# Optimization experiments

Hardware: AMD Instinct MI355X
Metric: run time of the kernel (lower is better)

## Reference

```python
import jax, jax.numpy as jnp
import numpy as np

B, N, L, E, U, G, R, D, C = 64, 50000, 8, 100000, 20000, 20000, 64, 16, 2


def setup_inputs() -> dict:
    rng = np.random.default_rng(0)
    key = jax.random.key(0)
    ks = jax.random.split(key, 10)
    # index structures (duplicate-free where the torch code assumes uniqueness)
    gene_map = jnp.asarray(rng.choice(N, G, replace=False).astype(np.int32))
    dst_unique = jnp.stack([jnp.asarray(rng.choice(N, U, replace=False).astype(np.int32)) for _ in range(L)])
    root_ids = jnp.asarray(rng.choice(N, R, replace=False).astype(np.int32))
    src = jax.random.randint(ks[0], (L, E), 0, N, dtype=jnp.int32)
    dst_pos = jax.random.randint(ks[1], (L, E), 0, U, dtype=jnp.int32)
    # data and parameters
    X_gene_batch = jax.random.normal(ks[2], (B, G), jnp.float32)
    w_in = jax.random.normal(ks[3], (D,), jnp.float32) * 0.5   # Linear(1, d) weight
    b_in = jax.random.normal(ks[4], (D,), jnp.float32) * 0.1
    W = jax.random.normal(ks[5], (L, D, D), jnp.float32) * (1.0 / np.sqrt(D))  # xavier-ish
    bias = jnp.zeros((N, D), jnp.float32)
    W_head = jax.random.normal(ks[6], (C, R * D), jnp.float32) * (1.0 / np.sqrt(R * D))
    b_head = jnp.zeros((C,), jnp.float32)
    return {
        "X_gene_batch": X_gene_batch, "w_in": w_in, "b_in": b_in, "W": W,
        "bias": bias, "W_head": W_head, "b_head": b_head,
        "gene_map": gene_map, "src": src, "dst_pos": dst_pos,
        "dst_unique": dst_unique, "root_ids": root_ids,
    }


def reference(X_gene_batch, w_in, b_in, W, bias, W_head, b_head,
              gene_map, src, dst_pos, dst_unique, root_ids):
    Bn = X_gene_batch.shape[0]
    n_nodes, d = bias.shape
    n_layers = W.shape[0]
    u = dst_unique.shape[1]
    # _init_state_vector: h=0, scatter in_proj(X[...,None]) at gene_map
    gene_emb = X_gene_batch[..., None] * w_in + b_in          # [B, G, d]
    h = jnp.zeros((Bn, n_nodes, d), X_gene_batch.dtype)
    h = h.at[:, gene_map].set(gene_emb)
    for li in range(n_layers):
        h_src = h[:, src[li]]                                  # gather [B, E, d]
        msg = jnp.einsum('bed,df->bef', h_src, W[li])          # small dxd matmul
        agg = jnp.zeros((Bn, u, d), h.dtype).at[:, dst_pos[li]].add(msg)  # scatter-add
        h_dst = jnp.tanh(agg + bias[dst_unique[li]][None])     # bias lookup + tanh (dropout=0)
        h = h.at[:, dst_unique[li]].set(h_dst)                 # write back
    feat = h[:, root_ids].reshape(Bn, -1)                      # roots_concat readout
    return feat @ W_head.T + b_head                            # [B, C]
```

## Files before the change

### kernel.cpp

```cpp
#include <hip/hip_runtime.h>
#include <hip/hip_fp16.h>
#include <cmath>

constexpr int B_ = 64, N_ = 50000, L_ = 8, E_ = 100000, U_ = 20000, G_ = 20000, R_ = 64, D_ = 16, C_ = 2;
constexpr int EPL_ = E_ + 3 * U_ + 4096;
constexpr int EPLG_ = EPL_ / 4 + 64;
constexpr int GPW = 4;
constexpr int BC = 64;
constexpr int F = BC * 2;
constexpr int GCAP = EPL_ / 4;
constexpr int SW = (GCAP + GPW - 1) / GPW;


__device__ __forceinline__ float tanh_fast(float x) {
  float e = __expf(2.0f * x);
  return 1.0f - 2.0f * __builtin_amdgcn_rcpf(e + 1.0f);
}


__global__ __launch_bounds__(256) void hist_kernel(
    const int* __restrict__ dst_pos, int* __restrict__ cnt,
    int* __restrict__ rank) {
  int e = blockIdx.x * 256 + threadIdx.x;
  int li = blockIdx.y;
  if (e >= E_) return;
  rank[li * E_ + e] = atomicAdd(&cnt[li * U_ + dst_pos[li * E_ + e]], 1);
}

__global__ __launch_bounds__(1024) void scan_kernel(
    const int* __restrict__ cnt, int* __restrict__ offs) {
  __shared__ int sums[1024];
  int li = blockIdx.x, t = threadIdx.x;
  int base = t * 20;
  int v[20];
  int s = 0;
#pragma unroll
  for (int i = 0; i < 20; ++i) {
    int idx = base + i;
    int c = (idx < U_) ? cnt[li * U_ + idx] : -1;
    int pc = (c < 0) ? 0 : ((c == 0) ? 4 : ((c + 3) & ~3));
    v[i] = s;
    s += pc;
  }
  sums[t] = s;
  __syncthreads();
  for (int off = 1; off < 1024; off <<= 1) {
    int o = (t >= off) ? sums[t - off] : 0;
    __syncthreads();
    sums[t] += o;
    __syncthreads();
  }
  int excl = sums[t] - s;
#pragma unroll
  for (int i = 0; i < 20; ++i) {
    int idx = base + i;
    if (idx < U_) offs[li * (U_ + 1) + idx] = excl + v[i];
  }
  if (t == 1023) offs[li * (U_ + 1) + U_] = sums[1023];
}

__global__ __launch_bounds__(256) void scatter_kernel(
    const int* __restrict__ dst_pos, const int* __restrict__ src,
    const int* __restrict__ offs, const int* __restrict__ rank,
    int* __restrict__ ssrc) {
  int e = blockIdx.x * 256 + threadIdx.x;
  int li = blockIdx.y;
  if (e >= E_) return;
  int u = dst_pos[li * E_ + e];
  int p = offs[li * (U_ + 1) + u] + rank[li * E_ + e];
  ssrc[(size_t)li * EPL_ + p] = src[li * E_ + e];
}

__global__ __launch_bounds__(256) void pad_fill_ug_k(
    const int* __restrict__ cnt, const int* __restrict__ offs,
    int* __restrict__ ssrc, int* __restrict__ ug) {
  int t = blockIdx.x * 256 + threadIdx.x;
  if (t < L_ * U_) {
    int li = t / U_, u = t % U_;
    int start = offs[li * (U_ + 1) + u];
    int end = start + cnt[li * U_ + u];
    int pend = offs[li * (U_ + 1) + u + 1];
    int* sp = ssrc + (size_t)li * EPL_;
    for (int p = end; p < pend; ++p) sp[p] = N_;
    int* ugp = ug + (size_t)li * EPLG_;
    for (int g = start >> 2; g < (pend >> 2); ++g) ugp[g] = u;
  } else {
    int t2 = t - L_ * U_;
    int li = t2 >> 8, j = t2 & 255;
    if (li < L_) {
      int* sp = ssrc + (size_t)li * EPL_;
      int ptot = offs[li * (U_ + 1) + U_];
      int pos = ptot + j;
      if (pos < EPL_) sp[pos] = N_;
      sp[EPL_ - 256 + j] = N_;
    }
  }
}


__global__ __launch_bounds__(256) void gene_init_k(
    const float* __restrict__ X, const float* __restrict__ w_in,
    const float* __restrict__ b_in, const int* __restrict__ gene_map,
    float4* __restrict__ h4) {
  int t = blockIdx.x * 256 + threadIdx.x;
  if (t >= G_ * BC) return;
  int b = t % BC;
  int g = t / BC;
  float x = X[b * G_ + g];
  int node = gene_map[g];
  float4 out[2];
  __half2* oh = reinterpret_cast<__half2*>(out);
#pragma unroll
  for (int k = 0; k < 8; ++k) {
    float r0 = fmaf(x, w_in[2 * k], b_in[2 * k]);
    float r1 = fmaf(x, w_in[2 * k + 1], b_in[2 * k + 1]);
    oh[k] = __float22half2_rn(make_float2(r0, r1));
  }
  h4[(size_t)node * F + b * 2] = out[0];
  h4[(size_t)node * F + b * 2 + 1] = out[1];
}

__global__ __launch_bounds__(256) void gather_k(
    const float4* __restrict__ h4, const int* __restrict__ ug,
    const int* __restrict__ ssrc, float4* __restrict__ agg4, int li) {
  int tid = threadIdx.x;
  int lane = tid & 63;
  int wv = __builtin_amdgcn_readfirstlane(blockIdx.x * 4 + (tid >> 6));
  int g0 = wv * GPW, gend = g0 + GPW;
  const int* ugp = ug + (size_t)li * EPLG_;
  const int* sp = ssrc + (size_t)li * EPL_;

  int prevU = (g0 == 0) ? -2 : ugp[g0 - 1];
  int g = g0;
  while (g < gend && ugp[g] == prevU) ++g;
  if (g >= gend) return;
  int curU = ugp[g];
  if (curU < 0) return;

  int uend = ugp[gend - 1];
  int gstop;
  if (uend < 0) {
    gstop = g;
    while (ugp[gstop] >= 0) ++gstop;
  } else {
    gstop = gend;
    while (ugp[gstop] == uend) ++gstop;
  }

  __half2 acc[2][2][4];
  const __half2 z = __half2half2(__float2half(0.f));
#pragma unroll
  for (int j = 0; j < 2; ++j)
#pragma unroll
    for (int r = 0; r < 2; ++r)
#pragma unroll
      for (int k = 0; k < 4; ++k) acc[j][r][k] = z;

  auto flushu = [&](int u) {
#pragma unroll
    for (int r = 0; r < 2; ++r) {
      float4 outv;
      __half2* ov = reinterpret_cast<__half2*>(&outv);
#pragma unroll
      for (int k = 0; k < 4; ++k) {
        float2 f0 = __half22float2(acc[0][r][k]);
        float2 f1 = __half22float2(acc[1][r][k]);
        ov[k] = __float22half2_rn(make_float2(f0.x + f1.x, f0.y + f1.y));
      }
      agg4[(size_t)u * F + lane + r * 64] = outv;
    }
#pragma unroll
    for (int j = 0; j < 2; ++j)
#pragma unroll
      for (int r = 0; r < 2; ++r)
#pragma unroll
        for (int k = 0; k < 4; ++k) acc[j][r][k] = z;
  };

  auto loadRows = [&](float4 (&v)[4][2], int4 id) {
    v[0][0] = h4[(size_t)id.x * F + lane]; v[0][1] = h4[(size_t)id.x * F + lane + 64];
    v[1][0] = h4[(size_t)id.y * F + lane]; v[1][1] = h4[(size_t)id.y * F + lane + 64];
    v[2][0] = h4[(size_t)id.z * F + lane]; v[2][1] = h4[(size_t)id.z * F + lane + 64];
    v[3][0] = h4[(size_t)id.w * F + lane]; v[3][1] = h4[(size_t)id.w * F + lane + 64];
  };
  auto accum = [&](const float4 (&v)[4][2]) {
#pragma unroll
    for (int j = 0; j < 4; ++j)
#pragma unroll
      for (int r = 0; r < 2; ++r) {
        const __half2* p = reinterpret_cast<const __half2*>(&v[j][r]);
#pragma unroll
        for (int k = 0; k < 4; ++k)
          acc[j & 1][r][k] = __hadd2(acc[j & 1][r][k], p[k]);
      }
  };

  auto CLG = [&](int q) { return (q < GCAP) ? q : GCAP - 1; };

  int4 id0 = *(const int4*)(sp + 4 * g);
  int4 id1 = *(const int4*)(sp + 4 * CLG(g + 1));
  int4 idP = *(const int4*)(sp + 4 * CLG(g + 2));
  int4 idQ = *(const int4*)(sp + 4 * CLG(g + 3));
  int4 idR;
  int nuA = ugp[g + 1];
  int nuB = ugp[CLG(g + 1) + 1];
  int nuC = ugp[CLG(g + 2) + 1];

  float4 va[4][2], vb[4][2], vc[4][2];
  loadRows(va, id0);
  loadRows(vb, id1);

#define PHASE(VACC, VLD, IDLD, IDPF, NUCUR)          \
  {                                                  \
    loadRows(VLD, IDLD);                             \
    IDPF = *(const int4*)(sp + 4 * CLG(g + 4));      \
    int nuCur = NUCUR;                               \
    NUCUR = ugp[CLG(g + 3) + 1];                     \
    accum(VACC);                                     \
    if (nuCur != curU) {                             \
      flushu(curU);                                  \
      if (g + 1 >= gstop) return;                    \
      curU = nuCur;                                  \
    }                                                \
    ++g;                                             \
  }

  for (;;) {
    PHASE(va, vc, idP, idR, nuA)
    PHASE(vb, va, idQ, idP, nuB)
    PHASE(vc, vb, idR, idQ, nuC)
  }
#undef PHASE
}

__global__ __launch_bounds__(256) void dense_k(
    const float4* __restrict__ agg4, const float* __restrict__ W,
    const float* __restrict__ bias, const int* __restrict__ dst_unique,
    float4* __restrict__ h4, int li) {
  __shared__ float Wlds[256];
  int tid = threadIdx.x;
  Wlds[tid] = W[li * 256 + tid];
  __syncthreads();
  int u = __builtin_amdgcn_readfirstlane(blockIdx.x * 4 + (tid >> 6));
  int b = tid & 63;
  float4 c0 = agg4[(size_t)u * F + b * 2];
  float4 c1 = agg4[(size_t)u * F + b * 2 + 1];
  float a[16];
  {
    const __half2* p0 = reinterpret_cast<const __half2*>(&c0);
    const __half2* p1 = reinterpret_cast<const __half2*>(&c1);
#pragma unroll
    for (int k = 0; k < 4; ++k) {
      float2 f0 = __half22float2(p0[k]);
      float2 f1 = __half22float2(p1[k]);
      a[2 * k] = f0.x; a[2 * k + 1] = f0.y;
      a[8 + 2 * k] = f1.x; a[8 + 2 * k + 1] = f1.y;
    }
  }
  float m[16];
#pragma unroll
  for (int j = 0; j < 16; ++j) m[j] = 0.f;
#pragma unroll
  for (int d = 0; d < 16; ++d) {
    float s = a[d];
    const float4* wr = (const float4*)&Wlds[d * 16];
    float4 w0 = wr[0], w1 = wr[1], w2 = wr[2], w3 = wr[3];
    m[0] = fmaf(s, w0.x, m[0]);  m[1] = fmaf(s, w0.y, m[1]);
    m[2] = fmaf(s, w0.z, m[2]);  m[3] = fmaf(s, w0.w, m[3]);
    m[4] = fmaf(s, w1.x, m[4]);  m[5] = fmaf(s, w1.y, m[5]);
    m[6] = fmaf(s, w1.z, m[6]);  m[7] = fmaf(s, w1.w, m[7]);
    m[8] = fmaf(s, w2.x, m[8]);  m[9] = fmaf(s, w2.y, m[9]);
    m[10] = fmaf(s, w2.z, m[10]); m[11] = fmaf(s, w2.w, m[11]);
    m[12] = fmaf(s, w3.x, m[12]); m[13] = fmaf(s, w3.y, m[13]);
    m[14] = fmaf(s, w3.z, m[14]); m[15] = fmaf(s, w3.w, m[15]);
  }
  int node = dst_unique[li * U_ + u];
  const float4* bp = (const float4*)(bias + (size_t)node * 16);
  float4 b0 = bp[0], b1 = bp[1], b2 = bp[2], b3 = bp[3];
  float bb[16] = {b0.x, b0.y, b0.z, b0.w, b1.x, b1.y, b1.z, b1.w,
                  b2.x, b2.y, b2.z, b2.w, b3.x, b3.y, b3.z, b3.w};
  float4 o0, o1;
  __half2* ov0 = reinterpret_cast<__half2*>(&o0);
  __half2* ov1 = reinterpret_cast<__half2*>(&o1);
#pragma unroll
  for (int k = 0; k < 4; ++k) {
    ov0[k] = __float22half2_rn(make_float2(tanh_fast(m[2 * k] + bb[2 * k]),
                                           tanh_fast(m[2 * k + 1] + bb[2 * k + 1])));
    ov1[k] = __float22half2_rn(make_float2(tanh_fast(m[8 + 2 * k] + bb[8 + 2 * k]),
                                           tanh_fast(m[8 + 2 * k + 1] + bb[8 + 2 * k + 1])));
  }
  h4[(size_t)node * F + b * 2] = o0;
  h4[(size_t)node * F + b * 2 + 1] = o1;
}

__global__ __launch_bounds__(64) void head_k(
    const float4* __restrict__ h4, const float* __restrict__ W_head,
    const float* __restrict__ b_head, const int* __restrict__ root_ids,
    float* __restrict__ out) {
  int bl = blockIdx.x;
  int r = threadIdx.x;
  int node = root_ids[r];
  float4 p0 = h4[(size_t)node * F + bl * 2];
  float4 p1 = h4[(size_t)node * F + bl * 2 + 1];
  float v[16];
  const __half2* ph0 = reinterpret_cast<const __half2*>(&p0);
  const __half2* ph1 = reinterpret_cast<const __half2*>(&p1);
#pragma unroll
  for (int k = 0; k < 4; ++k) {
    float2 f0 = __half22float2(ph0[k]);
    float2 f1 = __half22float2(ph1[k]);
    v[2 * k] = f0.x; v[2 * k + 1] = f0.y;
    v[8 + 2 * k] = f1.x; v[8 + 2 * k + 1] = f1.y;
  }
  float acc0 = 0.f, acc1 = 0.f;
#pragma unroll
  for (int d = 0; d < 16; ++d) {
    acc0 = fmaf(v[d], W_head[r * 16 + d], acc0);
    acc1 = fmaf(v[d], W_head[1024 + r * 16 + d], acc1);
  }
  for (int off = 32; off; off >>= 1) {
    acc0 += __shfl_down(acc0, off, 64);
    acc1 += __shfl_down(acc1, off, 64);
  }
  if (r == 0) {
    out[bl * 2 + 0] = acc0 + b_head[0];
    out[bl * 2 + 1] = acc1 + b_head[1];
  }
}

__global__ void zero_out_k(float* out, int n) {
  int t = blockIdx.x * 256 + threadIdx.x;
  if (t < n) out[t] = 0.f;
}


static size_t need_bytes() {
  return (size_t)(N_ + 1) * F * 16 + (size_t)U_ * F * 16 +
         (size_t)L_ * U_ * 4 +
         (size_t)L_ * (U_ + 1) * 4 +
         (size_t)L_ * E_ * 4 +
         (size_t)L_ * EPL_ * 4 +
         (size_t)L_ * EPLG_ * 4;
}

extern "C" void kernel_launch(void* const* d_in, const int* in_sizes, int n_in,
                              void* d_out, int out_size, void* d_ws, size_t ws_size,
                              hipStream_t stream) {
  if (ws_size < need_bytes()) {
    zero_out_k<<<(out_size + 255) / 256, 256, 0, stream>>>((float*)d_out, out_size);
    return;
  }
  const float* X = (const float*)d_in[0];
  const float* w_in = (const float*)d_in[1];
  const float* b_in = (const float*)d_in[2];
  const float* W = (const float*)d_in[3];
  const float* bias = (const float*)d_in[4];
  const float* W_head = (const float*)d_in[5];
  const float* b_head = (const float*)d_in[6];
  const int* gene_map = (const int*)d_in[7];
  const int* src = (const int*)d_in[8];
  const int* dst_pos = (const int*)d_in[9];
  const int* dst_unique = (const int*)d_in[10];
  const int* root_ids = (const int*)d_in[11];
  float* out = (float*)d_out;

  const size_t h_bytes = (size_t)(N_ + 1) * F * 16;
  const size_t agg_bytes = (size_t)U_ * F * 16;
  const size_t cnt_bytes = (size_t)L_ * U_ * 4;
  const size_t offs_bytes = (size_t)L_ * (U_ + 1) * 4;
  const size_t rank_bytes = (size_t)L_ * E_ * 4;
  const size_t ssrc_bytes = (size_t)L_ * EPL_ * 4;
  const size_t ug_bytes = (size_t)L_ * EPLG_ * 4;

  char* ws = (char*)d_ws;
  float4* h4 = (float4*)ws;
  float4* agg4 = (float4*)(ws + h_bytes);
  int* cnt = (int*)(ws + h_bytes + agg_bytes);
  int* offs = (int*)(ws + h_bytes + agg_bytes + cnt_bytes);
  int* rank = (int*)(ws + h_bytes + agg_bytes + cnt_bytes + offs_bytes);
  int* ssrc = (int*)(ws + h_bytes + agg_bytes + cnt_bytes + offs_bytes + rank_bytes);
  int* ug = (int*)(ws + h_bytes + agg_bytes + cnt_bytes + offs_bytes + rank_bytes + ssrc_bytes);

  hipMemsetAsync(cnt, 0, cnt_bytes, stream);
  hipMemsetAsync(ug, 0xFF, ug_bytes, stream);
  hipMemsetAsync(h4, 0, h_bytes, stream);
  dim3 egrid((E_ + 255) / 256, L_);
  hist_kernel<<<egrid, 256, 0, stream>>>(dst_pos, cnt, rank);
  scan_kernel<<<L_, 1024, 0, stream>>>(cnt, offs);
  scatter_kernel<<<egrid, 256, 0, stream>>>(dst_pos, src, offs, rank, ssrc);
  const int pf_grid = (L_ * U_ + L_ * 256 + 255) / 256;
  pad_fill_ug_k<<<pf_grid, 256, 0, stream>>>(cnt, offs, ssrc, ug);

  gene_init_k<<<(G_ * BC + 255) / 256, 256, 0, stream>>>(X, w_in, b_in, gene_map, h4);

  const int gather_grid = (SW + 3) / 4;
  const int dense_grid = U_ * BC / 256;
  for (int li = 0; li < L_; ++li) {
    gather_k<<<gather_grid, 256, 0, stream>>>(h4, ug, ssrc, agg4, li);
    dense_k<<<dense_grid, 256, 0, stream>>>(agg4, W, bias, dst_unique, h4, li);
  }

  head_k<<<BC, 64, 0, stream>>>(h4, W_head, b_head, root_ids, out);
}
```

Baseline: 681.9 us.

## Use versioned arena layout with fused gather-dense kernel and batch halves

Replaces the in-place node-state buffer with an append-only arena where each layer writes its outputs to fresh rows. Source indices are remapped ahead of time to the physical row holding the latest version of each node. This removes the large memset of the full state buffer and the separate aggregation buffer, and lets gather, the 16x16 matmul, bias and tanh run in one kernel per layer. The batch is processed in two halves of 32, which halves row width so the working set fits cache better but doubles the layer launches. Gather granularity also grows to 8 groups per wave. It adds remap preprocessing and more launches, and the old path is kept as a fallback for small workspaces.

```diff
diff --git a/kernel.cpp b/kernel.cpp
--- a/kernel.cpp
+++ b/kernel.cpp
@@ -5,12 +5,17 @@
 constexpr int B_ = 64, N_ = 50000, L_ = 8, E_ = 100000, U_ = 20000, G_ = 20000, R_ = 64, D_ = 16, C_ = 2;
 constexpr int EPL_ = E_ + 3 * U_ + 4096;
 constexpr int EPLG_ = EPL_ / 4 + 64;
-constexpr int GPW = 4;
+constexpr int GPW = 8;
+constexpr int GCAP = EPL_ / 4;
+constexpr int SW = (GCAP + GPW - 1) / GPW;
+
 constexpr int BC = 64;
 constexpr int F = BC * 2;
-constexpr int GCAP = EPL_ / 4;
-constexpr int SW = (GCAP + GPW - 1) / GPW;
-
+
+constexpr int HBC = 32;
+constexpr int FH = HBC * 2;
+constexpr int DST0 = 1 + G_;
+constexpr int AROWS = DST0 + L_ * U_;
 
 __device__ __forceinline__ float tanh_fast(float x) {
   float e = __expf(2.0f * x);
@@ -98,117 +103,42 @@
 }
 
 
-__global__ __launch_bounds__(256) void gene_init_k(
-    const float* __restrict__ X, const float* __restrict__ w_in,
-    const float* __restrict__ b_in, const int* __restrict__ gene_map,
-    float4* __restrict__ h4) {
+__global__ __launch_bounds__(256) void mark_k(
+    const int* __restrict__ dst_unique, const int* __restrict__ gene_map,
+    int* __restrict__ wmask, int* __restrict__ posarr, int* __restrict__ lw0) {
   int t = blockIdx.x * 256 + threadIdx.x;
-  if (t >= G_ * BC) return;
-  int b = t % BC;
-  int g = t / BC;
-  float x = X[b * G_ + g];
-  int node = gene_map[g];
-  float4 out[2];
-  __half2* oh = reinterpret_cast<__half2*>(out);
-#pragma unroll
-  for (int k = 0; k < 8; ++k) {
-    float r0 = fmaf(x, w_in[2 * k], b_in[2 * k]);
-    float r1 = fmaf(x, w_in[2 * k + 1], b_in[2 * k + 1]);
-    oh[k] = __float22half2_rn(make_float2(r0, r1));
-  }
-  h4[(size_t)node * F + b * 2] = out[0];
-  h4[(size_t)node * F + b * 2 + 1] = out[1];
-}
-
-__global__ __launch_bounds__(256) void gather_k(
-    const float4* __restrict__ h4, const int* __restrict__ ug,
-    const int* __restrict__ ssrc, float4* __restrict__ agg4, int li) {
-  int tid = threadIdx.x;
-  int lane = tid & 63;
-  int wv = __builtin_amdgcn_readfirstlane(blockIdx.x * 4 + (tid >> 6));
-  int g0 = wv * GPW, gend = g0 + GPW;
-  const int* ugp = ug + (size_t)li * EPLG_;
-  const int* sp = ssrc + (size_t)li * EPL_;
-
-  int prevU = (g0 == 0) ? -2 : ugp[g0 - 1];
-  int g = g0;
-  while (g < gend && ugp[g] == prevU) ++g;
-  if (g >= gend) return;
-  int curU = ugp[g];
-  if (curU < 0) return;
-
-  int uend = ugp[gend - 1];
-  int gstop;
-  if (uend < 0) {
-    gstop = g;
-    while (ugp[gstop] >= 0) ++gstop;
+  if (t < L_ * U_) {
+    int li = t / U_, u = t % U_;
+    int n = dst_unique[t];
+    posarr[li * N_ + n] = u;
+    atomicOr(&wmask[n], 1 << li);
   } else {
-    gstop = gend;
-    while (ugp[gstop] == uend) ++gstop;
-  }
-
-  __half2 acc[2][2][4];
-  const __half2 z = __half2half2(__float2half(0.f));
-#pragma unroll
-  for (int j = 0; j < 2; ++j)
-#pragma unroll
-    for (int r = 0; r < 2; ++r)
-#pragma unroll
-      for (int k = 0; k < 4; ++k) acc[j][r][k] = z;
-
-  auto flushu = [&](int u) {
-#pragma unroll
-    for (int r = 0; r < 2; ++r) {
-      float4 outv;
-      __half2* ov = reinterpret_cast<__half2*>(&outv);
-#pragma unroll
-      for (int k = 0; k < 4; ++k) {
-        float2 f0 = __half22float2(acc[0][r][k]);
-        float2 f1 = __half22float2(acc[1][r][k]);
-        ov[k] = __float22half2_rn(make_float2(f0.x + f1.x, f0.y + f1.y));
-      }
-      agg4[(size_t)u * F + lane + r * 64] = outv;
-    }
-#pragma unroll
-    for (int j = 0; j < 2; ++j)
-#pragma unroll
-      for (int r = 0; r < 2; ++r)
-#pragma unroll
-        for (int k = 0; k < 4; ++k) acc[j][r][k] = z;
-  };
-
-  auto loadRows = [&](float4 (&v)[4][2], int4 id) {
-    v[0][0] = h4[(size_t)id.x * F + lane]; v[0][1] = h4[(size_t)id.x * F + lane + 64];
-    v[1][0] = h4[(size_t)id.y * F + lane]; v[1][1] = h4[(size_t)id.y * F + lane + 64];
-    v[2][0] = h4[(size_t)id.z * F + lane]; v[2][1] = h4[(size_t)id.z * F + lane + 64];
-    v[3][0] = h4[(size_t)id.w * F + lane]; v[3][1] = h4[(size_t)id.w * F + lane + 64];
-  };
-  auto accum = [&](const float4 (&v)[4][2]) {
-#pragma unroll
-    for (int j = 0; j < 4; ++j)
-#pragma unroll
-      for (int r = 0; r < 2; ++r) {
-        const __half2* p = reinterpret_cast<const __half2*>(&v[j][r]);
-#pragma unroll
-        for (int k = 0; k < 4; ++k)
-          acc[j & 1][r][k] = __hadd2(acc[j & 1][r][k], p[k]);
-      }
-  };
-
-  auto CLG = [&](int q) { return (q < GCAP) ? q : GCAP - 1; };
-
-  int4 id0 = *(const int4*)(sp + 4 * g);
-  int4 id1 = *(const int4*)(sp + 4 * CLG(g + 1));
-  int4 idP = *(const int4*)(sp + 4 * CLG(g + 2));
-  int4 idQ = *(const int4*)(sp + 4 * CLG(g + 3));
-  int4 idR;
-  int nuA = ugp[g + 1];
-  int nuB = ugp[CLG(g + 1) + 1];
-  int nuC = ugp[CLG(g + 2) + 1];
-
-  float4 va[4][2], vb[4][2], vc[4][2];
-  loadRows(va, id0);
-  loadRows(vb, id1);
+    int g = t - L_ * U_;
+    if (g < G_) lw0[gene_map[g]] = 1 + g;
+  }
+}
+
+__global__ __launch_bounds__(256) void remap_k(
+    const int* __restrict__ offs, const int* __restrict__ wmask,
+    const int* __restrict__ posarr, const int* __restrict__ lw0,
+    int* __restrict__ ssrc) {
+  int p = blockIdx.x * 256 + threadIdx.x;
+  int li = blockIdx.y;
+  if (p >= EPL_) return;
+  int ptot = offs[li * (U_ + 1) + U_];
+  if (p >= ptot + 256 && p < EPL_ - 256) return;
+  int* sp = ssrc + (size_t)li * EPL_;
+  int s = sp[p];
+  int m = wmask[s] & ((1 << li) - 1);
+  int phys;
+  if (m) {
+    int lj = 31 - __clz(m);
+    phys = DST0 + lj * U_ + posarr[lj * N_ + s];
+  } else {
+    phys = lw0[s];
+  }
+  sp[p] = phys;
+}
 
 #define PHASE(VACC, VLD, IDLD, IDPF, NUCUR)          \
   {                                                  \
@@ -225,15 +155,325 @@
     ++g;                                             \
   }
 
+
+__global__ __launch_bounds__(256) void gene_a(
+    const float* __restrict__ X, const float* __restrict__ w_in,
+    const float* __restrict__ b_in, float4* __restrict__ h4, int half) {
+  int t = blockIdx.x * 256 + threadIdx.x;
+  if (t >= G_ * HBC) return;
+  int b = t % HBC;
+  int g = t / HBC;
+  float x = X[(half * HBC + b) * G_ + g];
+  float4 out[2];
+  __half2* oh = reinterpret_cast<__half2*>(out);
+#pragma unroll
+  for (int k = 0; k < 8; ++k) {
+    float r0 = fmaf(x, w_in[2 * k], b_in[2 * k]);
+    float r1 = fmaf(x, w_in[2 * k + 1], b_in[2 * k + 1]);
+    oh[k] = __float22half2_rn(make_float2(r0, r1));
+  }
+  h4[(size_t)(1 + g) * FH + b * 2] = out[0];
+  h4[(size_t)(1 + g) * FH + b * 2 + 1] = out[1];
+}
+
+__global__ __launch_bounds__(256, 2) void gfused_a(
+    const float4* __restrict__ h4, const int* __restrict__ ug,
+    const int* __restrict__ ssrc, const float* __restrict__ W,
+    const float* __restrict__ bias, const int* __restrict__ dst_unique,
+    float4* __restrict__ o4, int li) {
+  __shared__ float Wlds[256];
+  int tid = threadIdx.x;
+  Wlds[tid] = W[li * 256 + tid];
+  __syncthreads();
+  int lane = tid & 63;
+  int dh = lane & 1;
+  int wv = __builtin_amdgcn_readfirstlane(blockIdx.x * 4 + (tid >> 6));
+  const int* ugp = ug + (size_t)li * EPLG_;
+  const int* sp = ssrc + (size_t)li * EPL_;
+  const int* du = dst_unique + (size_t)li * U_;
+
+  int g0 = wv * GPW, gend = g0 + GPW;
+  int prevU = (g0 == 0) ? -2 : ugp[g0 - 1];
+  int g = g0;
+  while (g < gend && ugp[g] == prevU) ++g;
+  if (g >= gend) return;
+  int curU = ugp[g];
+  if (curU < 0) return;
+  int uend = ugp[gend - 1];
+  int gstop;
+  if (uend < 0) {
+    gstop = g;
+    while (ugp[gstop] >= 0) ++gstop;
+  } else {
+    gstop = gend;
+    while (ugp[gstop] == uend) ++gstop;
+  }
+
+  __half2 acc[2][4];
+  const __half2 z = __half2half2(__float2half(0.f));
+#pragma unroll
+  for (int j = 0; j < 2; ++j)
+#pragma unroll
+    for (int k = 0; k < 4; ++k) acc[j][k] = z;
+
+  auto flushu = [&](int u) {
+    int node = du[u];
+    float biasv[8];
+    {
+      const float4* bp = (const float4*)(bias + (size_t)node * 16 + dh * 8);
+      float4 q0 = bp[0], q1 = bp[1];
+      biasv[0] = q0.x; biasv[1] = q0.y; biasv[2] = q0.z; biasv[3] = q0.w;
+      biasv[4] = q1.x; biasv[5] = q1.y; biasv[6] = q1.z; biasv[7] = q1.w;
+    }
+    float a8[8];
+#pragma unroll
+    for (int k = 0; k < 4; ++k) {
+      float2 f0 = __half22float2(acc[0][k]);
+      float2 f1 = __half22float2(acc[1][k]);
+      __half2 hv = __float22half2_rn(make_float2(f0.x + f1.x, f0.y + f1.y));
+      float2 fa = __half22float2(hv);
+      a8[2 * k] = fa.x; a8[2 * k + 1] = fa.y;
+    }
+    float pm[16];
+#pragma unroll
+    for (int j = 0; j < 16; ++j) pm[j] = 0.f;
+#pragma unroll
+    for (int dd = 0; dd < 8; ++dd) {
+      float s = a8[dd];
+      const float4* wr = (const float4*)&Wlds[(dh * 8 + dd) * 16];
+      float4 w0 = wr[0], w1 = wr[1], w2 = wr[2], w3 = wr[3];
+      pm[0] = fmaf(s, w0.x, pm[0]);  pm[1] = fmaf(s, w0.y, pm[1]);
+      pm[2] = fmaf(s, w0.z, pm[2]);  pm[3] = fmaf(s, w0.w, pm[3]);
+      pm[4] = fmaf(s, w1.x, pm[4]);  pm[5] = fmaf(s, w1.y, pm[5]);
+      pm[6] = fmaf(s, w1.z, pm[6]);  pm[7] = fmaf(s, w1.w, pm[7]);
+      pm[8] = fmaf(s, w2.x, pm[8]);  pm[9] = fmaf(s, w2.y, pm[9]);
+      pm[10] = fmaf(s, w2.z, pm[10]); pm[11] = fmaf(s, w2.w, pm[11]);
+      pm[12] = fmaf(s, w3.x, pm[12]); pm[13] = fmaf(s, w3.y, pm[13]);
+      pm[14] = fmaf(s, w3.z, pm[14]); pm[15] = fmaf(s, w3.w, pm[15]);
+    }
+    float m8[8];
+#pragma unroll
+    for (int jj = 0; jj < 8; ++jj) {
+      float s0 = pm[jj] + __shfl_xor(pm[jj], 1, 64);
+      float s1 = pm[8 + jj] + __shfl_xor(pm[8 + jj], 1, 64);
+      m8[jj] = dh ? s1 : s0;
+    }
+    float4 outv;
+    __half2* ov = reinterpret_cast<__half2*>(&outv);
+#pragma unroll
+    for (int k = 0; k < 4; ++k) {
+      ov[k] = __float22half2_rn(
+          make_float2(tanh_fast(m8[2 * k] + biasv[2 * k]),
+                      tanh_fast(m8[2 * k + 1] + biasv[2 * k + 1])));
+    }
+    o4[(size_t)(DST0 + li * U_ + u) * FH + lane] = outv;
+#pragma unroll
+    for (int j = 0; j < 2; ++j)
+#pragma unroll
+      for (int k = 0; k < 4; ++k) acc[j][k] = z;
+  };
+
+  auto loadRows = [&](float4 (&v)[4], int4 id) {
+    v[0] = h4[(size_t)id.x * FH + lane];
+    v[1] = h4[(size_t)id.y * FH + lane];
+    v[2] = h4[(size_t)id.z * FH + lane];
+    v[3] = h4[(size_t)id.w * FH + lane];
+  };
+  auto accum = [&](const float4 (&v)[4]) {
+#pragma unroll
+    for (int j = 0; j < 4; ++j) {
+      const __half2* p = reinterpret_cast<const __half2*>(&v[j]);
+#pragma unroll
+      for (int k = 0; k < 4; ++k)
+        acc[j & 1][k] = __hadd2(acc[j & 1][k], p[k]);
+    }
+  };
+  auto CLG = [&](int q) { return (q < GCAP) ? q : GCAP - 1; };
+
+  int4 id0 = *(const int4*)(sp + 4 * g);
+  int4 id1 = *(const int4*)(sp + 4 * CLG(g + 1));
+  int4 idP = *(const int4*)(sp + 4 * CLG(g + 2));
+  int4 idQ = *(const int4*)(sp + 4 * CLG(g + 3));
+  int4 idR;
+  int nuA = ugp[g + 1];
+  int nuB = ugp[CLG(g + 1) + 1];
+  int nuC = ugp[CLG(g + 2) + 1];
+
+  float4 va[4], vb[4], vc[4];
+  loadRows(va, id0);
+  loadRows(vb, id1);
+
   for (;;) {
     PHASE(va, vc, idP, idR, nuA)
     PHASE(vb, va, idQ, idP, nuB)
     PHASE(vc, vb, idR, idQ, nuC)
   }
+}
+
+__global__ __launch_bounds__(64) void head_a(
+    const float4* __restrict__ h4, const float* __restrict__ W_head,
+    const float* __restrict__ b_head, const int* __restrict__ root_ids,
+    const int* __restrict__ wmask, const int* __restrict__ posarr,
+    const int* __restrict__ lw0, int half, float* __restrict__ out) {
+  int bl = blockIdx.x;
+  int r = threadIdx.x;
+  int node = root_ids[r];
+  int m = wmask[node];
+  int phys;
+  if (m) {
+    int lj = 31 - __clz(m);
+    phys = DST0 + lj * U_ + posarr[lj * N_ + node];
+  } else {
+    phys = lw0[node];
+  }
+  float4 p0 = h4[(size_t)phys * FH + bl * 2];
+  float4 p1 = h4[(size_t)phys * FH + bl * 2 + 1];
+  float v[16];
+  const __half2* ph0 = reinterpret_cast<const __half2*>(&p0);
+  const __half2* ph1 = reinterpret_cast<const __half2*>(&p1);
+#pragma unroll
+  for (int k = 0; k < 4; ++k) {
+    float2 f0 = __half22float2(ph0[k]);
+    float2 f1 = __half22float2(ph1[k]);
+    v[2 * k] = f0.x; v[2 * k + 1] = f0.y;
+    v[8 + 2 * k] = f1.x; v[8 + 2 * k + 1] = f1.y;
+  }
+  float acc0 = 0.f, acc1 = 0.f;
+#pragma unroll
+  for (int d = 0; d < 16; ++d) {
+    acc0 = fmaf(v[d], W_head[r * 16 + d], acc0);
+    acc1 = fmaf(v[d], W_head[1024 + r * 16 + d], acc1);
+  }
+  for (int off = 32; off; off >>= 1) {
+    acc0 += __shfl_down(acc0, off, 64);
+    acc1 += __shfl_down(acc1, off, 64);
+  }
+  if (r == 0) {
+    int gb = half * HBC + bl;
+    out[gb * 2 + 0] = acc0 + b_head[0];
+    out[gb * 2 + 1] = acc1 + b_head[1];
+  }
+}
+
+
+__global__ __launch_bounds__(256) void gene_c(
+    const float* __restrict__ X, const float* __restrict__ w_in,
+    const float* __restrict__ b_in, const int* __restrict__ gene_map,
+    float4* __restrict__ h4) {
+  int t = blockIdx.x * 256 + threadIdx.x;
+  if (t >= G_ * BC) return;
+  int b = t % BC;
+  int g = t / BC;
+  float x = X[b * G_ + g];
+  int node = gene_map[g];
+  float4 out[2];
+  __half2* oh = reinterpret_cast<__half2*>(out);
+#pragma unroll
+  for (int k = 0; k < 8; ++k) {
+    float r0 = fmaf(x, w_in[2 * k], b_in[2 * k]);
+    float r1 = fmaf(x, w_in[2 * k + 1], b_in[2 * k + 1]);
+    oh[k] = __float22half2_rn(make_float2(r0, r1));
+  }
+  h4[(size_t)node * F + b * 2] = out[0];
+  h4[(size_t)node * F + b * 2 + 1] = out[1];
+}
+
+__global__ __launch_bounds__(256, 2) void gather_c(
+    const float4* __restrict__ h4, const int* __restrict__ ug,
+    const int* __restrict__ ssrc, float4* __restrict__ agg4, int li) {
+  int tid = threadIdx.x;
+  int lane = tid & 63;
+  int wv = __builtin_amdgcn_readfirstlane(blockIdx.x * 4 + (tid >> 6));
+  const int* ugp = ug + (size_t)li * EPLG_;
+  const int* sp = ssrc + (size_t)li * EPL_;
+
+  int g0 = wv * GPW, gend = g0 + GPW;
+  int prevU = (g0 == 0) ? -2 : ugp[g0 - 1];
+  int g = g0;
+  while (g < gend && ugp[g] == prevU) ++g;
+  if (g >= gend) return;
+  int curU = ugp[g];
+  if (curU < 0) return;
+  int uend = ugp[gend - 1];
+  int gstop;
+  if (uend < 0) {
+    gstop = g;
+    while (ugp[gstop] >= 0) ++gstop;
+  } else {
+    gstop = gend;
+    while (ugp[gstop] == uend) ++gstop;
+  }
+
+  __half2 acc[2][2][4];
+  const __half2 z = __half2half2(__float2half(0.f));
+#pragma unroll
+  for (int j = 0; j < 2; ++j)
+#pragma unroll
+    for (int r = 0; r < 2; ++r)
+#pragma unroll
+      for (int k = 0; k < 4; ++k) acc[j][r][k] = z;
+
+  auto flushu = [&](int u) {
+#pragma unroll
+    for (int r = 0; r < 2; ++r) {
+      float4 outv;
+      __half2* ov = reinterpret_cast<__half2*>(&outv);
+#pragma unroll
+      for (int k = 0; k < 4; ++k) {
+        float2 f0 = __half22float2(acc[0][r][k]);
+        float2 f1 = __half22float2(acc[1][r][k]);
+        ov[k] = __float22half2_rn(make_float2(f0.x + f1.x, f0.y + f1.y));
+      }
+      agg4[(size_t)u * F + lane + r * 64] = outv;
+    }
+#pragma unroll
+    for (int j = 0; j < 2; ++j)
+#pragma unroll
+      for (int r = 0; r < 2; ++r)
+#pragma unroll
+        for (int k = 0; k < 4; ++k) acc[j][r][k] = z;
+  };
+  auto loadRows = [&](float4 (&v)[4][2], int4 id) {
+    v[0][0] = h4[(size_t)id.x * F + lane]; v[0][1] = h4[(size_t)id.x * F + lane + 64];
+    v[1][0] = h4[(size_t)id.y * F + lane]; v[1][1] = h4[(size_t)id.y * F + lane + 64];
+    v[2][0] = h4[(size_t)id.z * F + lane]; v[2][1] = h4[(size_t)id.z * F + lane + 64];
+    v[3][0] = h4[(size_t)id.w * F + lane]; v[3][1] = h4[(size_t)id.w * F + lane + 64];
+  };
+  auto accum = [&](const float4 (&v)[4][2]) {
+#pragma unroll
+    for (int j = 0; j < 4; ++j)
+#pragma unroll
+      for (int r = 0; r < 2; ++r) {
+        const __half2* p = reinterpret_cast<const __half2*>(&v[j][r]);
+#pragma unroll
+        for (int k = 0; k < 4; ++k)
+          acc[j & 1][r][k] = __hadd2(acc[j & 1][r][k], p[k]);
+      }
+  };
+  auto CLG = [&](int q) { return (q < GCAP) ? q : GCAP - 1; };
+
+  int4 id0 = *(const int4*)(sp + 4 * g);
+  int4 id1 = *(const int4*)(sp + 4 * CLG(g + 1));
+  int4 idP = *(const int4*)(sp + 4 * CLG(g + 2));
+  int4 idQ = *(const int4*)(sp + 4 * CLG(g + 3));
+  int4 idR;
+  int nuA = ugp[g + 1];
+  int nuB = ugp[CLG(g + 1) + 1];
+  int nuC = ugp[CLG(g + 2) + 1];
+
+  float4 va[4][2], vb[4][2], vc[4][2];
+  loadRows(va, id0);
+  loadRows(vb, id1);
+
+  for (;;) {
+    PHASE(va, vc, idP, idR, nuA)
+    PHASE(vb, va, idQ, idP, nuB)
+    PHASE(vc, vb, idR, idQ, nuC)
+  }
+}
 #undef PHASE
-}
-
-__global__ __launch_bounds__(256) void dense_k(
+
+__global__ __launch_bounds__(256) void dense_c(
     const float4* __restrict__ agg4, const float* __restrict__ W,
     const float* __restrict__ bias, const int* __restrict__ dst_unique,
     float4* __restrict__ h4, int li) {
@@ -293,7 +533,7 @@
   h4[(size_t)node * F + b * 2 + 1] = o1;
 }
 
-__global__ __launch_bounds__(64) void head_k(
+__global__ __launch_bounds__(64) void head_c(
     const float4* __restrict__ h4, const float* __restrict__ W_head,
     const float* __restrict__ b_head, const int* __restrict__ root_ids,
     float* __restrict__ out) {
@@ -334,22 +574,25 @@
 }
 
 
-static size_t need_bytes() {
-  return (size_t)(N_ + 1) * F * 16 + (size_t)U_ * F * 16 +
-         (size_t)L_ * U_ * 4 +
+static size_t csr_aux_bytes() {
+  return (size_t)L_ * U_ * 4 +
          (size_t)L_ * (U_ + 1) * 4 +
          (size_t)L_ * E_ * 4 +
          (size_t)L_ * EPL_ * 4 +
          (size_t)L_ * EPLG_ * 4;
 }
+static size_t arena_bytes() {
+  return (size_t)AROWS * FH * 16 + csr_aux_bytes() +
+         (size_t)2 * (N_ + 1) * 4 +
+         (size_t)L_ * N_ * 4;
+}
+static size_t classic_bytes() {
+  return (size_t)(N_ + 1) * F * 16 + (size_t)U_ * F * 16 + csr_aux_bytes();
+}
 
 extern "C" void kernel_launch(void* const* d_in, const int* in_sizes, int n_in,
                               void* d_out, int out_size, void* d_ws, size_t ws_size,
                               hipStream_t stream) {
-  if (ws_size < need_bytes()) {
-    zero_out_k<<<(out_size + 255) / 256, 256, 0, stream>>>((float*)d_out, out_size);
-    return;
-  }
   const float* X = (const float*)d_in[0];
   const float* w_in = (const float*)d_in[1];
   const float* b_in = (const float*)d_in[2];
@@ -364,41 +607,75 @@
   const int* root_ids = (const int*)d_in[11];
   float* out = (float*)d_out;
 
-  const size_t h_bytes = (size_t)(N_ + 1) * F * 16;
-  const size_t agg_bytes = (size_t)U_ * F * 16;
-  const size_t cnt_bytes = (size_t)L_ * U_ * 4;
-  const size_t offs_bytes = (size_t)L_ * (U_ + 1) * 4;
-  const size_t rank_bytes = (size_t)L_ * E_ * 4;
-  const size_t ssrc_bytes = (size_t)L_ * EPL_ * 4;
-  const size_t ug_bytes = (size_t)L_ * EPLG_ * 4;
-
-  char* ws = (char*)d_ws;
-  float4* h4 = (float4*)ws;
-  float4* agg4 = (float4*)(ws + h_bytes);
-  int* cnt = (int*)(ws + h_bytes + agg_bytes);
-  int* offs = (int*)(ws + h_bytes + agg_bytes + cnt_bytes);
-  int* rank = (int*)(ws + h_bytes + agg_bytes + cnt_bytes + offs_bytes);
-  int* ssrc = (int*)(ws + h_bytes + agg_bytes + cnt_bytes + offs_bytes + rank_bytes);
-  int* ug = (int*)(ws + h_bytes + agg_bytes + cnt_bytes + offs_bytes + rank_bytes + ssrc_bytes);
-
-  hipMemsetAsync(cnt, 0, cnt_bytes, stream);
-  hipMemsetAsync(ug, 0xFF, ug_bytes, stream);
-  hipMemsetAsync(h4, 0, h_bytes, stream);
   dim3 egrid((E_ + 255) / 256, L_);
-  hist_kernel<<<egrid, 256, 0, stream>>>(dst_pos, cnt, rank);
-  scan_kernel<<<L_, 1024, 0, stream>>>(cnt, offs);
-  scatter_kernel<<<egrid, 256, 0, stream>>>(dst_pos, src, offs, rank, ssrc);
   const int pf_grid = (L_ * U_ + L_ * 256 + 255) / 256;
-  pad_fill_ug_k<<<pf_grid, 256, 0, stream>>>(cnt, offs, ssrc, ug);
-
-  gene_init_k<<<(G_ * BC + 255) / 256, 256, 0, stream>>>(X, w_in, b_in, gene_map, h4);
-
   const int gather_grid = (SW + 3) / 4;
-  const int dense_grid = U_ * BC / 256;
-  for (int li = 0; li < L_; ++li) {
-    gather_k<<<gather_grid, 256, 0, stream>>>(h4, ug, ssrc, agg4, li);
-    dense_k<<<dense_grid, 256, 0, stream>>>(agg4, W, bias, dst_unique, h4, li);
-  }
-
-  head_k<<<BC, 64, 0, stream>>>(h4, W_head, b_head, root_ids, out);
-}
+
+  if (ws_size >= arena_bytes()) {
+    char* ws = (char*)d_ws;
+    float4* arena = (float4*)ws;
+    size_t off = (size_t)AROWS * FH * 16;
+    int* cnt = (int*)(ws + off);    off += (size_t)L_ * U_ * 4;
+    int* offs = (int*)(ws + off);   off += (size_t)L_ * (U_ + 1) * 4;
+    int* rank = (int*)(ws + off);   off += (size_t)L_ * E_ * 4;
+    int* ssrc = (int*)(ws + off);   off += (size_t)L_ * EPL_ * 4;
+    int* ug = (int*)(ws + off);     off += (size_t)L_ * EPLG_ * 4;
+    int* wmask = (int*)(ws + off);  off += (size_t)(N_ + 1) * 4;
+    int* lw0 = (int*)(ws + off);    off += (size_t)(N_ + 1) * 4;
+    int* posarr = (int*)(ws + off);
+
+    hipMemsetAsync(cnt, 0, (size_t)L_ * U_ * 4, stream);
+    hipMemsetAsync(ug, 0xFF, (size_t)L_ * EPLG_ * 4, stream);
+    hipMemsetAsync(wmask, 0, (size_t)2 * (N_ + 1) * 4, stream);
+    hipMemsetAsync(arena, 0, (size_t)FH * 16, stream);
+
+    hist_kernel<<<egrid, 256, 0, stream>>>(dst_pos, cnt, rank);
+    scan_kernel<<<L_, 1024, 0, stream>>>(cnt, offs);
+    scatter_kernel<<<egrid, 256, 0, stream>>>(dst_pos, src, offs, rank, ssrc);
+    pad_fill_ug_k<<<pf_grid, 256, 0, stream>>>(cnt, offs, ssrc, ug);
+    mark_k<<<(L_ * U_ + G_ + 255) / 256, 256, 0, stream>>>(dst_unique, gene_map,
+                                                           wmask, posarr, lw0);
+    dim3 rgrid((EPL_ + 255) / 256, L_);
+    remap_k<<<rgrid, 256, 0, stream>>>(offs, wmask, posarr, lw0, ssrc);
+
+    for (int half = 0; half < 2; ++half) {
+      gene_a<<<(G_ * HBC + 255) / 256, 256, 0, stream>>>(X, w_in, b_in, arena,
+                                                         half);
+      for (int li = 0; li < L_; ++li) {
+        gfused_a<<<gather_grid, 256, 0, stream>>>(arena, ug, ssrc, W, bias,
+                                                  dst_unique, arena, li);
+      }
+      head_a<<<HBC, 64, 0, stream>>>(arena, W_head, b_head, root_ids, wmask,
+                                     posarr, lw0, half, out);
+    }
+  } else if (ws_size >= classic_bytes()) {
+    const size_t h_bytes = (size_t)(N_ + 1) * F * 16;
+    const size_t agg_bytes = (size_t)U_ * F * 16;
+    char* ws = (char*)d_ws;
+    float4* h4 = (float4*)ws;
+    float4* agg4 = (float4*)(ws + h_bytes);
+    size_t off = h_bytes + agg_bytes;
+    int* cnt = (int*)(ws + off);  off += (size_t)L_ * U_ * 4;
+    int* offs = (int*)(ws + off); off += (size_t)L_ * (U_ + 1) * 4;
+    int* rank = (int*)(ws + off); off += (size_t)L_ * E_ * 4;
+    int* ssrc = (int*)(ws + off); off += (size_t)L_ * EPL_ * 4;
+    int* ug = (int*)(ws + off);
+
+    hipMemsetAsync(cnt, 0, (size_t)L_ * U_ * 4, stream);
+    hipMemsetAsync(ug, 0xFF, (size_t)L_ * EPLG_ * 4, stream);
+    hipMemsetAsync(h4, 0, h_bytes, stream);
+    hist_kernel<<<egrid, 256, 0, stream>>>(dst_pos, cnt, rank);
+    scan_kernel<<<L_, 1024, 0, stream>>>(cnt, offs);
+    scatter_kernel<<<egrid, 256, 0, stream>>>(dst_pos, src, offs, rank, ssrc);
+    pad_fill_ug_k<<<pf_grid, 256, 0, stream>>>(cnt, offs, ssrc, ug);
+    gene_c<<<(G_ * BC + 255) / 256, 256, 0, stream>>>(X, w_in, b_in, gene_map, h4);
+    const int dense_grid = U_ * BC / 256;
+    for (int li = 0; li < L_; ++li) {
+      gather_c<<<gather_grid, 256, 0, stream>>>(h4, ug, ssrc, agg4, li);
+      dense_c<<<dense_grid, 256, 0, stream>>>(agg4, W, bias, dst_unique, h4, li);
+    }
+    head_c<<<BC, 64, 0, stream>>>(h4, W_head, b_head, root_ids, out);
+  } else {
+    zero_out_k<<<(out_size + 255) / 256, 256, 0, stream>>>(out, out_size);
+  }
+}
```

After: 550.7 us. -19.2%, faster.
